# Optimization experiments

Hardware: AMD Instinct MI355X
Metric: run time of the kernel (lower is better)

## Reference

```python
import jax, jax.numpy as jnp
import numpy as np

N_HEADS = 8
ITER = 3


def setup_inputs() -> dict:
    key = jax.random.key(0)
    ks = jax.random.split(key, 9)
    B, L, D = 2, 2048, 512
    s = 1.0 / np.sqrt(D)
    return {
        "queries": jax.random.normal(ks[0], (B, L, D), jnp.float32),
        "keys": jax.random.normal(ks[1], (B, L, D), jnp.float32),
        "values": jax.random.normal(ks[2], (B, L, D), jnp.float32),
        "Wq": jax.random.normal(ks[3], (D, D), jnp.float32) * s,
        "bq": jax.random.normal(ks[4], (D,), jnp.float32) * s,
        "Wk": jax.random.normal(ks[5], (D, D), jnp.float32) * s,
        "bk": jax.random.normal(ks[6], (D,), jnp.float32) * s,
        "Wv": jax.random.normal(ks[7], (D, D), jnp.float32) * s,
        "bv": jax.random.normal(ks[8], (D,), jnp.float32) * s,
    }


def reference(queries, keys, values, Wq, bq, Wk, bk, Wv, bv):
    B, L, D = queries.shape
    S = keys.shape[1]
    H = N_HEADS
    E = D // H
    q = (queries @ Wq + bq).reshape(B, L, H, E)
    k = (keys @ Wk + bk).reshape(B, S, H, E)
    v = (values @ Wv + bv).reshape(B, S, H, E)

    attn_list = []
    vals_accum = jnp.zeros((B, S, H, E), dtype=q.dtype)
    for i in range(ITER):
        stride = i + 1
        tmp_q = q[:, ::stride]  # (B, L_i, H, E) strided query gather
        attn = jnp.einsum('blhe,bshe->bhls', tmp_q, k)  # (B,H,L_i,S)
        attn_list.append(attn)
        att = jax.nn.softmax(attn, axis=-1)
        # dropout is identity in eval mode
        # 'bhls,bshe->bshe' == values scaled by column-sum of attention over l
        colsum = att.sum(axis=2)  # (B,H,S)
        vals_accum = vals_accum + v * colsum.transpose(0, 2, 1)[..., None]
    final_values = vals_accum / ITER  # mean over the ITER branches
    out = final_values.reshape(B, S, H * E)
    return (out, *attn_list)
```

## Files before the change

### kernel.cpp

```cpp
#include <hip/hip_runtime.h>


typedef short s16x8 __attribute__((ext_vector_type(8)));
typedef float f32x4 __attribute__((ext_vector_type(4)));
typedef unsigned short u16;

#define MFMA16(a, b, c) __builtin_amdgcn_mfma_f32_16x16x32_bf16((a), (b), (c), 0, 0, 0)

__device__ __forceinline__ u16 f32_to_bf16(float f) {
  unsigned u = __builtin_bit_cast(unsigned, f);
  unsigned r = u + 0x7fffu + ((u >> 16) & 1u);
  return (u16)(r >> 16);
}
__device__ __forceinline__ void split1(float x, u16& h, u16& l) {
  h = f32_to_bf16(x);
  l = f32_to_bf16(x - __builtin_bit_cast(float, (unsigned)h << 16));
}

__global__ __launch_bounds__(256) void split_all(const float* __restrict__ in_q,
                                                 const float* __restrict__ in_k,
                                                 const float* __restrict__ in_v,
                                                 const float* __restrict__ Wq,
                                                 const float* __restrict__ Wk,
                                                 const float* __restrict__ Wv,
                                                 u16* __restrict__ Xsplit,
                                                 u16* __restrict__ Wsplit) {
  int which = blockIdx.y;
  int bx = blockIdx.x;
  if (bx < 1024) {
    const float* X = (which == 0) ? in_q : (which == 1) ? in_k : in_v;
    u16* Xh = Xsplit + (size_t)which * 2 * 2097152;
    u16* Xl = Xh + 2097152;
    int t = bx * 256 + threadIdx.x;
    int lane = t & 63;
    int kc = (t >> 6) & 15;
    int mt = t >> 10;
    int lr = lane & 15, g = lane >> 4;
    const float* p = X + (size_t)(mt * 16 + lr) * 512 + kc * 32 + g * 8;
    float4 a = *(const float4*)p;
    float4 b = *(const float4*)(p + 4);
    float x[8] = {a.x, a.y, a.z, a.w, b.x, b.y, b.z, b.w};
    s16x8 hv, lv;
#pragma unroll
    for (int j = 0; j < 8; ++j) {
      u16 hh, ll;
      split1(x[j], hh, ll);
      hv[j] = (short)hh;
      lv[j] = (short)ll;
    }
    size_t off = (size_t)t * 8;
    *(s16x8*)(Xh + off) = hv;
    *(s16x8*)(Xl + off) = lv;
  } else {
    const float* W = (which == 0) ? Wq : (which == 1) ? Wk : Wv;
    u16* Wh = Wsplit + (size_t)which * 2 * 262144;
    u16* Wl = Wh + 262144;
    int t = (bx - 1024) * 256 + threadIdx.x;
    int lane = t & 63;
    int kc = (t >> 6) & 15;
    int nt = t >> 10;
    int lr = lane & 15, g = lane >> 4;
    s16x8 hv, lv;
#pragma unroll
    for (int j = 0; j < 8; ++j) {
      float x = W[(size_t)(kc * 32 + g * 8 + j) * 512 + nt * 16 + lr];
      u16 hh, ll;
      split1(x, hh, ll);
      hv[j] = (short)hh;
      lv[j] = (short)ll;
    }
    size_t off = (size_t)t * 8;
    *(s16x8*)(Wh + off) = hv;
    *(s16x8*)(Wl + off) = lv;
  }
}

__global__ __launch_bounds__(256) void proj_gemm3(const u16* __restrict__ Xsplit,
                                                  const u16* __restrict__ Wsplit,
                                                  const float* __restrict__ bq,
                                                  const float* __restrict__ bk,
                                                  const float* __restrict__ bv,
                                                  float* __restrict__ vout,
                                                  u16* __restrict__ qh,
                                                  u16* __restrict__ ql,
                                                  u16* __restrict__ kh,
                                                  u16* __restrict__ kl) {
  int z = blockIdx.z;
  const u16* Xh = Xsplit + (size_t)z * 2 * 2097152;
  const u16* Xl = Xh + 2097152;
  const u16* Wh = Wsplit + (size_t)z * 2 * 262144;
  const u16* Wl = Wh + 262144;
  const float* bias = (z == 0) ? bq : (z == 1) ? bk : bv;
  u16* Yhi = (z == 0) ? qh : kh;
  u16* Ylo = (z == 0) ? ql : kl;

  int tid = threadIdx.x;
  int wid = tid >> 6, lane = tid & 63;
  int wr = wid >> 1, wc = wid & 1;
  int mtb = blockIdx.y * 4 + wr * 2;
  int ntb = blockIdx.x * 4 + wc * 2;

  f32x4 zero = {0.f, 0.f, 0.f, 0.f};
  f32x4 acc[2][2];
#pragma unroll
  for (int m = 0; m < 2; ++m)
#pragma unroll
    for (int n = 0; n < 2; ++n) acc[m][n] = zero;

  for (int kc = 0; kc < 16; ++kc) {
    s16x8 ah[2], al[2], bh[2], bl[2];
#pragma unroll
    for (int m = 0; m < 2; ++m) {
      size_t off = ((size_t)((mtb + m) * 16 + kc) * 64 + lane) * 8;
      ah[m] = *(const s16x8*)(Xh + off);
      al[m] = *(const s16x8*)(Xl + off);
    }
#pragma unroll
    for (int n = 0; n < 2; ++n) {
      size_t off = ((size_t)((ntb + n) * 16 + kc) * 64 + lane) * 8;
      bh[n] = *(const s16x8*)(Wh + off);
      bl[n] = *(const s16x8*)(Wl + off);
    }
#pragma unroll
    for (int m = 0; m < 2; ++m)
#pragma unroll
      for (int n = 0; n < 2; ++n) {
        acc[m][n] = MFMA16(ah[m], bh[n], acc[m][n]);
        acc[m][n] = MFMA16(ah[m], bl[n], acc[m][n]);
        acc[m][n] = MFMA16(al[m], bh[n], acc[m][n]);
      }
  }
  int cn = lane & 15, cr0 = (lane >> 4) * 4;
#pragma unroll
  for (int n = 0; n < 2; ++n) {
    int col = (ntb + n) * 16 + cn;
    float bv_ = bias[col];
#pragma unroll
    for (int m = 0; m < 2; ++m)
#pragma unroll
      for (int r = 0; r < 4; ++r) {
        int row = (mtb + m) * 16 + cr0 + r;
        float y = acc[m][n][r] + bv_;
        if (z == 2) {
          vout[(size_t)row * 512 + col] = y;
        } else {
          int b = row >> 11, l = row & 2047;
          int h = col >> 6, e = col & 63;
          int bh2 = b * 8 + h;
          int lt = l >> 4, lr2 = l & 15;
          int kc2 = e >> 5, g2 = (e >> 3) & 3, j2 = e & 7;
          size_t idx = ((((size_t)bh2 * 128 + lt) * 2 + kc2) * 64 + g2 * 16 + lr2) * 8 + j2;
          u16 hh, ll;
          split1(y, hh, ll);
          Yhi[idx] = hh;
          Ylo[idx] = ll;
        }
      }
  }
}

__global__ __launch_bounds__(512, 4) void attn_fused(const u16* __restrict__ qh,
                                                     const u16* __restrict__ ql,
                                                     const u16* __restrict__ kh,
                                                     const u16* __restrict__ kl,
                                                     float* __restrict__ a1,
                                                     float* __restrict__ a2,
                                                     float* __restrict__ a3,
                                                     float* __restrict__ partials) {
  int bh = blockIdx.y;
  int lblk = blockIdx.x;
  int tid = threadIdx.x, wid = tid >> 6, lane = tid & 63;

  s16x8 qhf[2], qlf[2];
#pragma unroll
  for (int kc = 0; kc < 2; ++kc) {
    size_t off = ((((size_t)bh * 128 + lblk) * 2 + kc) * 64 + lane) * 8;
    qhf[kc] = *(const s16x8*)(qh + off);
    qlf[kc] = *(const s16x8*)(ql + off);
  }

  f32x4 acc[16];
#pragma unroll
  for (int t = 0; t < 16; ++t) acc[t] = (f32x4){0.f, 0.f, 0.f, 0.f};

#pragma unroll
  for (int t = 0; t < 16; ++t) {
    int st = wid * 16 + t;
#pragma unroll
    for (int kc = 0; kc < 2; ++kc) {
      size_t off = ((((size_t)bh * 128 + st) * 2 + kc) * 64 + lane) * 8;
      s16x8 khf = *(const s16x8*)(kh + off);
      s16x8 klf = *(const s16x8*)(kl + off);
      acc[t] = MFMA16(qhf[kc], khf, acc[t]);
      acc[t] = MFMA16(qhf[kc], klf, acc[t]);
      acc[t] = MFMA16(qlf[kc], khf, acc[t]);
    }
  }

  int cn = lane & 15, rg = lane >> 4;
  int lbase = lblk * 16;
  float* A1 = a1 + (size_t)bh * 2048 * 2048;
  float* A2 = a2 + (size_t)bh * 1024 * 2048;
  float* A3 = a3 + (size_t)bh * 683 * 2048;
#pragma unroll
  for (int r = 0; r < 4; ++r) {
    int l = lbase + rg * 4 + r;
    float* p1 = A1 + (size_t)l * 2048 + wid * 256 + cn;
#pragma unroll
    for (int t = 0; t < 16; ++t) __builtin_nontemporal_store(acc[t][r], p1 + t * 16);
    if ((l & 1) == 0) {
      float* p2 = A2 + (size_t)(l >> 1) * 2048 + wid * 256 + cn;
#pragma unroll
      for (int t = 0; t < 16; ++t) __builtin_nontemporal_store(acc[t][r], p2 + t * 16);
    }
    if (l % 3 == 0) {
      float* p3 = A3 + (size_t)(l / 3) * 2048 + wid * 256 + cn;
#pragma unroll
      for (int t = 0; t < 16; ++t) __builtin_nontemporal_store(acc[t][r], p3 + t * 16);
    }
  }

  __shared__ float lred[16][8];
  float mrow[4];
#pragma unroll
  for (int r = 0; r < 4; ++r) {
    float m = acc[0][r];
#pragma unroll
    for (int t = 1; t < 16; ++t) m = fmaxf(m, acc[t][r]);
#pragma unroll
    for (int o = 1; o < 16; o <<= 1) m = fmaxf(m, __shfl_xor(m, o));
    mrow[r] = m;
  }
  if (cn == 0) {
#pragma unroll
    for (int r = 0; r < 4; ++r) lred[rg * 4 + r][wid] = mrow[r];
  }
  __syncthreads();
  float mfin[4];
#pragma unroll
  for (int r = 0; r < 4; ++r) {
    int rr = rg * 4 + r;
    float m = lred[rr][0];
#pragma unroll
    for (int w = 1; w < 8; ++w) m = fmaxf(m, lred[rr][w]);
    mfin[r] = m;
  }
  __syncthreads();

  float zrow[4] = {0.f, 0.f, 0.f, 0.f};
#pragma unroll
  for (int t = 0; t < 16; ++t) {
#pragma unroll
    for (int r = 0; r < 4; ++r) {
      float p = __expf(acc[t][r] - mfin[r]);
      acc[t][r] = p;
      zrow[r] += p;
    }
  }
#pragma unroll
  for (int r = 0; r < 4; ++r) {
#pragma unroll
    for (int o = 1; o < 16; o <<= 1) zrow[r] += __shfl_xor(zrow[r], o);
  }
  if (cn == 0) {
#pragma unroll
    for (int r = 0; r < 4; ++r) lred[rg * 4 + r][wid] = zrow[r];
  }
  __syncthreads();
  float winv[4];
#pragma unroll
  for (int r = 0; r < 4; ++r) {
    int rr = rg * 4 + r;
    int l = lbase + rr;
    float zs = lred[rr][0];
#pragma unroll
    for (int w = 1; w < 8; ++w) zs += lred[rr][w];
    float w_ = 1.f + (((l & 1) == 0) ? 1.f : 0.f) + ((l % 3 == 0) ? 1.f : 0.f);
    winv[r] = w_ / zs;
  }

  __shared__ float pcol[2048];
#pragma unroll
  for (int t = 0; t < 16; ++t) {
    float cs = acc[t][0] * winv[0] + acc[t][1] * winv[1] + acc[t][2] * winv[2] +
               acc[t][3] * winv[3];
    cs += __shfl_xor(cs, 16);
    cs += __shfl_xor(cs, 32);
    if (lane < 16) pcol[wid * 256 + t * 16 + cn] = cs;
  }
  __syncthreads();
  size_t pb = ((size_t)bh * 128 + lblk) * 2048;
#pragma unroll
  for (int i = 0; i < 4; ++i) partials[pb + i * 512 + tid] = pcol[i * 512 + tid];
}

__global__ __launch_bounds__(256) void reduce_partials(const float* __restrict__ partials,
                                                       float* __restrict__ csum) {
  int s = blockIdx.x * 256 + threadIdx.x;
  int bh = blockIdx.y;
  float acc = 0.f;
  for (int j = 0; j < 128; ++j) acc += partials[((size_t)(bh * 128 + j)) * 2048 + s];
  csum[(size_t)bh * 2048 + s] = acc;
}

__global__ __launch_bounds__(256) void final_out(const float* __restrict__ v,
                                                 const float* __restrict__ csum,
                                                 float* __restrict__ out) {
  int idx = blockIdx.x * 256 + threadIdx.x;
  int h = (idx >> 4) & 7;
  int s = (idx >> 7) & 2047;
  int b = idx >> 18;
  float4 vv = ((const float4*)v)[idx];
  float c = csum[(size_t)(b * 8 + h) * 2048 + s] * (1.f / 3.f);
  float4 o = {vv.x * c, vv.y * c, vv.z * c, vv.w * c};
  ((float4*)out)[idx] = o;
}

extern "C" void kernel_launch(void* const* d_in, const int* in_sizes, int n_in,
                              void* d_out, int out_size, void* d_ws, size_t ws_size,
                              hipStream_t stream) {
  const float* queries = (const float*)d_in[0];
  const float* keys    = (const float*)d_in[1];
  const float* values  = (const float*)d_in[2];
  const float* Wq = (const float*)d_in[3];
  const float* bq = (const float*)d_in[4];
  const float* Wk = (const float*)d_in[5];
  const float* bk = (const float*)d_in[6];
  const float* Wv = (const float*)d_in[7];
  const float* bv = (const float*)d_in[8];

  float* out = (float*)d_out;
  float* a1 = out + 2097152;
  float* a2 = a1 + 67108864;
  float* a3 = a2 + 33554432;

  float* ws = (float*)d_ws;
  float* v = ws;
  u16* qh = (u16*)(v + 2097152);
  u16* ql = qh + 2097152;
  u16* kh = ql + 2097152;
  u16* kl = kh + 2097152;
  u16* Wsplit = kl + 2097152;
  u16* Xsplit = Wsplit + 6 * 262144;
  float* partials = (float*)Xsplit;
  float* csum = (float*)Wsplit;

  split_all<<<dim3(1152, 3), 256, 0, stream>>>(queries, keys, values, Wq, Wk, Wv,
                                               Xsplit, Wsplit);

  proj_gemm3<<<dim3(8, 64, 3), 256, 0, stream>>>(Xsplit, Wsplit, bq, bk, bv, v,
                                                 qh, ql, kh, kl);

  attn_fused<<<dim3(128, 16), 512, 0, stream>>>(qh, ql, kh, kl, a1, a2, a3, partials);

  reduce_partials<<<dim3(8, 16), 256, 0, stream>>>(partials, csum);

  final_out<<<dim3(2048), 256, 0, stream>>>(v, csum, out);
}
```

Baseline: 195.2 us.

## Transpose MFMA operands for vectorized output stores; enlarge attention tiles to 32 rows

Swaps the A/B operands of the MFMAs in both the projection GEMM and the attention kernel, so each lane holds four consecutive columns of one row. Projection and attention-score outputs can then be written as 16-byte vector stores instead of scalar stores. The attention kernel now handles 32 query rows per 1024-thread block, which halves the partial-sum buffer and the reduction length, and the softmax reductions are reorganized around the new lane layout. In exchange, blocks are larger with more waves, so occupancy may drop and the column-sum shuffle reduction gets longer.

```diff
diff --git a/kernel.cpp b/kernel.cpp
--- a/kernel.cpp
+++ b/kernel.cpp
@@ -4,6 +4,7 @@
 typedef short s16x8 __attribute__((ext_vector_type(8)));
 typedef float f32x4 __attribute__((ext_vector_type(4)));
 typedef unsigned short u16;
+typedef unsigned short u16x4 __attribute__((ext_vector_type(4)));
 
 #define MFMA16(a, b, c) __builtin_amdgcn_mfma_f32_16x16x32_bf16((a), (b), (c), 0, 0, 0)
 
@@ -108,190 +109,201 @@
     for (int n = 0; n < 2; ++n) acc[m][n] = zero;
 
   for (int kc = 0; kc < 16; ++kc) {
-    s16x8 ah[2], al[2], bh[2], bl[2];
+    s16x8 xh[2], xl[2], wh[2], wl[2];
 #pragma unroll
     for (int m = 0; m < 2; ++m) {
       size_t off = ((size_t)((mtb + m) * 16 + kc) * 64 + lane) * 8;
-      ah[m] = *(const s16x8*)(Xh + off);
-      al[m] = *(const s16x8*)(Xl + off);
+      xh[m] = *(const s16x8*)(Xh + off);
+      xl[m] = *(const s16x8*)(Xl + off);
     }
 #pragma unroll
     for (int n = 0; n < 2; ++n) {
       size_t off = ((size_t)((ntb + n) * 16 + kc) * 64 + lane) * 8;
-      bh[n] = *(const s16x8*)(Wh + off);
-      bl[n] = *(const s16x8*)(Wl + off);
+      wh[n] = *(const s16x8*)(Wh + off);
+      wl[n] = *(const s16x8*)(Wl + off);
     }
 #pragma unroll
     for (int m = 0; m < 2; ++m)
 #pragma unroll
       for (int n = 0; n < 2; ++n) {
-        acc[m][n] = MFMA16(ah[m], bh[n], acc[m][n]);
-        acc[m][n] = MFMA16(ah[m], bl[n], acc[m][n]);
-        acc[m][n] = MFMA16(al[m], bh[n], acc[m][n]);
+        acc[m][n] = MFMA16(wh[n], xh[m], acc[m][n]);
+        acc[m][n] = MFMA16(wh[n], xl[m], acc[m][n]);
+        acc[m][n] = MFMA16(wl[n], xh[m], acc[m][n]);
       }
   }
-  int cn = lane & 15, cr0 = (lane >> 4) * 4;
-#pragma unroll
-  for (int n = 0; n < 2; ++n) {
-    int col = (ntb + n) * 16 + cn;
-    float bv_ = bias[col];
-#pragma unroll
-    for (int m = 0; m < 2; ++m)
-#pragma unroll
-      for (int r = 0; r < 4; ++r) {
-        int row = (mtb + m) * 16 + cr0 + r;
-        float y = acc[m][n][r] + bv_;
-        if (z == 2) {
-          vout[(size_t)row * 512 + col] = y;
-        } else {
-          int b = row >> 11, l = row & 2047;
-          int h = col >> 6, e = col & 63;
-          int bh2 = b * 8 + h;
-          int lt = l >> 4, lr2 = l & 15;
-          int kc2 = e >> 5, g2 = (e >> 3) & 3, j2 = e & 7;
-          size_t idx = ((((size_t)bh2 * 128 + lt) * 2 + kc2) * 64 + g2 * 16 + lr2) * 8 + j2;
+  int cn = lane & 15, rg = lane >> 4;
+#pragma unroll
+  for (int m = 0; m < 2; ++m) {
+    int row = (mtb + m) * 16 + cn;
+#pragma unroll
+    for (int n = 0; n < 2; ++n) {
+      int nc0 = (ntb + n) * 16 + rg * 4;
+      f32x4 b4 = *(const f32x4*)(bias + nc0);
+      f32x4 y;
+#pragma unroll
+      for (int r = 0; r < 4; ++r) y[r] = acc[m][n][r] + b4[r];
+      if (z == 2) {
+        *(f32x4*)(vout + (size_t)row * 512 + nc0) = y;
+      } else {
+        int b = row >> 11, l = row & 2047;
+        int h = nc0 >> 6;
+        int e0 = nc0 & 63;
+        int bh2 = b * 8 + h;
+        int lt = l >> 4, lr2 = l & 15;
+        int kc2 = e0 >> 5, g2 = (e0 >> 3) & 3, j0 = e0 & 7;
+        size_t idx = ((((size_t)bh2 * 128 + lt) * 2 + kc2) * 64 + g2 * 16 + lr2) * 8 + j0;
+        u16x4 hv, lv;
+#pragma unroll
+        for (int r = 0; r < 4; ++r) {
           u16 hh, ll;
-          split1(y, hh, ll);
-          Yhi[idx] = hh;
-          Ylo[idx] = ll;
+          split1(y[r], hh, ll);
+          hv[r] = hh;
+          lv[r] = ll;
         }
+        *(u16x4*)(Yhi + idx) = hv;
+        *(u16x4*)(Ylo + idx) = lv;
       }
-  }
-}
-
-__global__ __launch_bounds__(512, 4) void attn_fused(const u16* __restrict__ qh,
-                                                     const u16* __restrict__ ql,
-                                                     const u16* __restrict__ kh,
-                                                     const u16* __restrict__ kl,
-                                                     float* __restrict__ a1,
-                                                     float* __restrict__ a2,
-                                                     float* __restrict__ a3,
-                                                     float* __restrict__ partials) {
+    }
+  }
+}
+
+__global__ __launch_bounds__(1024, 4) void attn_fused(const u16* __restrict__ qh,
+                                                      const u16* __restrict__ ql,
+                                                      const u16* __restrict__ kh,
+                                                      const u16* __restrict__ kl,
+                                                      float* __restrict__ a1,
+                                                      float* __restrict__ a2,
+                                                      float* __restrict__ a3,
+                                                      float* __restrict__ partials) {
   int bh = blockIdx.y;
   int lblk = blockIdx.x;
   int tid = threadIdx.x, wid = tid >> 6, lane = tid & 63;
-
-  s16x8 qhf[2], qlf[2];
-#pragma unroll
-  for (int kc = 0; kc < 2; ++kc) {
-    size_t off = ((((size_t)bh * 128 + lblk) * 2 + kc) * 64 + lane) * 8;
-    qhf[kc] = *(const s16x8*)(qh + off);
-    qlf[kc] = *(const s16x8*)(ql + off);
-  }
-
-  f32x4 acc[16];
-#pragma unroll
-  for (int t = 0; t < 16; ++t) acc[t] = (f32x4){0.f, 0.f, 0.f, 0.f};
-
-#pragma unroll
-  for (int t = 0; t < 16; ++t) {
-    int st = wid * 16 + t;
+  int cn = lane & 15, rg = lane >> 4;
+  int lbase = lblk * 32;
+
+  f32x4 acc[2][8];
+#pragma unroll
+  for (int g = 0; g < 2; ++g)
+#pragma unroll
+    for (int t = 0; t < 8; ++t) acc[g][t] = (f32x4){0.f, 0.f, 0.f, 0.f};
+
+#pragma unroll
+  for (int g = 0; g < 2; ++g) {
+    s16x8 qhf[2], qlf[2];
 #pragma unroll
     for (int kc = 0; kc < 2; ++kc) {
-      size_t off = ((((size_t)bh * 128 + st) * 2 + kc) * 64 + lane) * 8;
-      s16x8 khf = *(const s16x8*)(kh + off);
-      s16x8 klf = *(const s16x8*)(kl + off);
-      acc[t] = MFMA16(qhf[kc], khf, acc[t]);
-      acc[t] = MFMA16(qhf[kc], klf, acc[t]);
-      acc[t] = MFMA16(qlf[kc], khf, acc[t]);
-    }
-  }
-
-  int cn = lane & 15, rg = lane >> 4;
-  int lbase = lblk * 16;
+      size_t off = ((((size_t)bh * 128 + lblk * 2 + g) * 2 + kc) * 64 + lane) * 8;
+      qhf[kc] = *(const s16x8*)(qh + off);
+      qlf[kc] = *(const s16x8*)(ql + off);
+    }
+#pragma unroll
+    for (int t = 0; t < 8; ++t) {
+      int st = wid * 8 + t;
+#pragma unroll
+      for (int kc = 0; kc < 2; ++kc) {
+        size_t off = ((((size_t)bh * 128 + st) * 2 + kc) * 64 + lane) * 8;
+        s16x8 khf = *(const s16x8*)(kh + off);
+        s16x8 klf = *(const s16x8*)(kl + off);
+        acc[g][t] = MFMA16(khf, qhf[kc], acc[g][t]);
+        acc[g][t] = MFMA16(khf, qlf[kc], acc[g][t]);
+        acc[g][t] = MFMA16(klf, qhf[kc], acc[g][t]);
+      }
+    }
+  }
+
   float* A1 = a1 + (size_t)bh * 2048 * 2048;
   float* A2 = a2 + (size_t)bh * 1024 * 2048;
   float* A3 = a3 + (size_t)bh * 683 * 2048;
-#pragma unroll
-  for (int r = 0; r < 4; ++r) {
-    int l = lbase + rg * 4 + r;
-    float* p1 = A1 + (size_t)l * 2048 + wid * 256 + cn;
-#pragma unroll
-    for (int t = 0; t < 16; ++t) __builtin_nontemporal_store(acc[t][r], p1 + t * 16);
+  int colb = wid * 128 + rg * 4;
+#pragma unroll
+  for (int g = 0; g < 2; ++g) {
+    int l = lbase + g * 16 + cn;
+    float* p1 = A1 + (size_t)l * 2048 + colb;
+#pragma unroll
+    for (int t = 0; t < 8; ++t)
+      __builtin_nontemporal_store(acc[g][t], (f32x4*)(p1 + t * 16));
     if ((l & 1) == 0) {
-      float* p2 = A2 + (size_t)(l >> 1) * 2048 + wid * 256 + cn;
-#pragma unroll
-      for (int t = 0; t < 16; ++t) __builtin_nontemporal_store(acc[t][r], p2 + t * 16);
+      float* p2 = A2 + (size_t)(l >> 1) * 2048 + colb;
+#pragma unroll
+      for (int t = 0; t < 8; ++t)
+        __builtin_nontemporal_store(acc[g][t], (f32x4*)(p2 + t * 16));
     }
     if (l % 3 == 0) {
-      float* p3 = A3 + (size_t)(l / 3) * 2048 + wid * 256 + cn;
-#pragma unroll
-      for (int t = 0; t < 16; ++t) __builtin_nontemporal_store(acc[t][r], p3 + t * 16);
-    }
-  }
-
-  __shared__ float lred[16][8];
-  float mrow[4];
-#pragma unroll
-  for (int r = 0; r < 4; ++r) {
-    float m = acc[0][r];
-#pragma unroll
-    for (int t = 1; t < 16; ++t) m = fmaxf(m, acc[t][r]);
-#pragma unroll
-    for (int o = 1; o < 16; o <<= 1) m = fmaxf(m, __shfl_xor(m, o));
-    mrow[r] = m;
-  }
-  if (cn == 0) {
-#pragma unroll
-    for (int r = 0; r < 4; ++r) lred[rg * 4 + r][wid] = mrow[r];
+      float* p3 = A3 + (size_t)(l / 3) * 2048 + colb;
+#pragma unroll
+      for (int t = 0; t < 8; ++t)
+        __builtin_nontemporal_store(acc[g][t], (f32x4*)(p3 + t * 16));
+    }
+  }
+
+  __shared__ float lred[32][17];
+  float mfin[2];
+#pragma unroll
+  for (int g = 0; g < 2; ++g) {
+    float m = acc[g][0][0];
+#pragma unroll
+    for (int t = 0; t < 8; ++t)
+#pragma unroll
+      for (int r = 0; r < 4; ++r) m = fmaxf(m, acc[g][t][r]);
+    m = fmaxf(m, __shfl_xor(m, 16));
+    m = fmaxf(m, __shfl_xor(m, 32));
+    if (lane < 16) lred[g * 16 + lane][wid] = m;
   }
   __syncthreads();
-  float mfin[4];
-#pragma unroll
-  for (int r = 0; r < 4; ++r) {
-    int rr = rg * 4 + r;
-    float m = lred[rr][0];
-#pragma unroll
-    for (int w = 1; w < 8; ++w) m = fmaxf(m, lred[rr][w]);
-    mfin[r] = m;
+#pragma unroll
+  for (int g = 0; g < 2; ++g) {
+    float m = lred[g * 16 + cn][0];
+#pragma unroll
+    for (int w = 1; w < 16; ++w) m = fmaxf(m, lred[g * 16 + cn][w]);
+    mfin[g] = m;
   }
   __syncthreads();
 
-  float zrow[4] = {0.f, 0.f, 0.f, 0.f};
-#pragma unroll
-  for (int t = 0; t < 16; ++t) {
-#pragma unroll
-    for (int r = 0; r < 4; ++r) {
-      float p = __expf(acc[t][r] - mfin[r]);
-      acc[t][r] = p;
-      zrow[r] += p;
-    }
-  }
-#pragma unroll
-  for (int r = 0; r < 4; ++r) {
-#pragma unroll
-    for (int o = 1; o < 16; o <<= 1) zrow[r] += __shfl_xor(zrow[r], o);
-  }
-  if (cn == 0) {
-#pragma unroll
-    for (int r = 0; r < 4; ++r) lred[rg * 4 + r][wid] = zrow[r];
+#pragma unroll
+  for (int g = 0; g < 2; ++g) {
+    float z = 0.f;
+#pragma unroll
+    for (int t = 0; t < 8; ++t)
+#pragma unroll
+      for (int r = 0; r < 4; ++r) {
+        float p = __expf(acc[g][t][r] - mfin[g]);
+        acc[g][t][r] = p;
+        z += p;
+      }
+    z += __shfl_xor(z, 16);
+    z += __shfl_xor(z, 32);
+    if (lane < 16) lred[g * 16 + lane][wid] = z;
   }
   __syncthreads();
-  float winv[4];
-#pragma unroll
-  for (int r = 0; r < 4; ++r) {
-    int rr = rg * 4 + r;
-    int l = lbase + rr;
-    float zs = lred[rr][0];
-#pragma unroll
-    for (int w = 1; w < 8; ++w) zs += lred[rr][w];
+  float winv[2];
+#pragma unroll
+  for (int g = 0; g < 2; ++g) {
+    float zs = lred[g * 16 + cn][0];
+#pragma unroll
+    for (int w = 1; w < 16; ++w) zs += lred[g * 16 + cn][w];
+    int l = lbase + g * 16 + cn;
     float w_ = 1.f + (((l & 1) == 0) ? 1.f : 0.f) + ((l % 3 == 0) ? 1.f : 0.f);
-    winv[r] = w_ / zs;
+    winv[g] = w_ / zs;
   }
 
   __shared__ float pcol[2048];
 #pragma unroll
-  for (int t = 0; t < 16; ++t) {
-    float cs = acc[t][0] * winv[0] + acc[t][1] * winv[1] + acc[t][2] * winv[2] +
-               acc[t][3] * winv[3];
-    cs += __shfl_xor(cs, 16);
-    cs += __shfl_xor(cs, 32);
-    if (lane < 16) pcol[wid * 256 + t * 16 + cn] = cs;
+  for (int t = 0; t < 8; ++t) {
+    f32x4 cs;
+#pragma unroll
+    for (int r = 0; r < 4; ++r)
+      cs[r] = acc[0][t][r] * winv[0] + acc[1][t][r] * winv[1];
+#pragma unroll
+    for (int o = 1; o < 16; o <<= 1) {
+#pragma unroll
+      for (int r = 0; r < 4; ++r) cs[r] += __shfl_xor(cs[r], o);
+    }
+    if (cn == 0) *(f32x4*)&pcol[wid * 128 + t * 16 + rg * 4] = cs;
   }
   __syncthreads();
-  size_t pb = ((size_t)bh * 128 + lblk) * 2048;
-#pragma unroll
-  for (int i = 0; i < 4; ++i) partials[pb + i * 512 + tid] = pcol[i * 512 + tid];
+  size_t pb = ((size_t)bh * 64 + lblk) * 2048;
+#pragma unroll
+  for (int i = 0; i < 2; ++i) partials[pb + i * 1024 + tid] = pcol[i * 1024 + tid];
 }
 
 __global__ __launch_bounds__(256) void reduce_partials(const float* __restrict__ partials,
@@ -299,7 +311,7 @@
   int s = blockIdx.x * 256 + threadIdx.x;
   int bh = blockIdx.y;
   float acc = 0.f;
-  for (int j = 0; j < 128; ++j) acc += partials[((size_t)(bh * 128 + j)) * 2048 + s];
+  for (int j = 0; j < 64; ++j) acc += partials[((size_t)(bh * 64 + j)) * 2048 + s];
   csum[(size_t)bh * 2048 + s] = acc;
 }
 
@@ -351,7 +363,7 @@
   proj_gemm3<<<dim3(8, 64, 3), 256, 0, stream>>>(Xsplit, Wsplit, bq, bk, bv, v,
                                                  qh, ql, kh, kl);
 
-  attn_fused<<<dim3(128, 16), 512, 0, stream>>>(qh, ql, kh, kl, a1, a2, a3, partials);
+  attn_fused<<<dim3(64, 16), 1024, 0, stream>>>(qh, ql, kh, kl, a1, a2, a3, partials);
 
   reduce_partials<<<dim3(8, 16), 256, 0, stream>>>(partials, csum);
 
```

After: 267.0 us. +36.8%, slower.
